# Optimization experiments

Hardware: AMD Instinct MI355X
Metric: run time of the kernel (lower is better)

## Reference

```python
import jax, jax.numpy as jnp
import numpy as np

NUM_HEADS = 16
ROPE_BASE = 10000.0


def _rope_cos_sin(seq_len, head_dim, dtype):
    inv_freq = 1.0 / (ROPE_BASE ** (jnp.arange(0, head_dim, 2, dtype=jnp.float32) / head_dim))
    freqs = jnp.arange(seq_len, dtype=jnp.float32)[:, None] * inv_freq[None, :]  # [L, hd/2]
    return jnp.cos(freqs).astype(dtype), jnp.sin(freqs).astype(dtype)


def _apply_rope(t, cos, sin):
    # t: [B, H, L, hd]; cos/sin: [L, hd/2] broadcast over B,H
    x1 = t[..., ::2]
    x2 = t[..., 1::2]
    r1 = x1 * cos - x2 * sin
    r2 = x1 * sin + x2 * cos
    return jnp.stack([r1, r2], axis=-1).reshape(t.shape)


def setup_inputs() -> dict:
    key = jax.random.key(0)
    k1, k2, k3 = jax.random.split(key, 3)
    B, L, D = 2, 2048, 1024
    x = jax.random.normal(k1, (B, L, D), dtype=jnp.float32)
    W_qkv = jax.random.normal(k2, (3 * D, D), dtype=jnp.float32) * (D ** -0.5)
    W_out = jax.random.normal(k3, (D, D), dtype=jnp.float32) * (D ** -0.5)
    return {"x": x, "W_qkv": W_qkv, "W_out": W_out}


def reference(x, W_qkv, W_out):
    B, L, D = x.shape
    H = NUM_HEADS
    hd = D // H
    scale = hd ** -0.5

    qkv = x @ W_qkv.T                              # [B, L, 3D]
    qkv = qkv.reshape(B, L, 3, H, hd)
    qkv = jnp.transpose(qkv, (2, 0, 3, 1, 4))      # [3, B, H, L, hd]
    q, k, v = qkv[0], qkv[1], qkv[2]

    cos, sin = _rope_cos_sin(L, hd, x.dtype)
    q = _apply_rope(q, cos, sin)
    k = _apply_rope(k, cos, sin)

    logits = jnp.einsum("bhqd,bhkd->bhqk", q, k) * scale
    attn = jax.nn.softmax(logits, axis=-1)         # dropout p=0.0 -> identity
    out = jnp.einsum("bhqk,bhkd->bhqd", attn, v)   # [B, H, L, hd]
    out = jnp.transpose(out, (0, 2, 1, 3)).reshape(B, L, D)
    return out @ W_out.T
```

## Files before the change

### kernel.cpp

```cpp
#include <hip/hip_runtime.h>
#include <hip/hip_bf16.h>
#include <stdint.h>


typedef __bf16 bf16x8 __attribute__((ext_vector_type(8)));
typedef float f32x4 __attribute__((ext_vector_type(4)));

__device__ __forceinline__ unsigned short f2bf(float f) {
  union { float f; unsigned int u; } v; v.f = f;
  unsigned int r = v.u + 0x7FFFu + ((v.u >> 16) & 1u);
  return (unsigned short)(r >> 16);
}
__device__ __forceinline__ float b2f(unsigned short u) {
  union { unsigned int u; float f; } v; v.u = ((unsigned int)u) << 16;
  return v.f;
}

__device__ __forceinline__ void gl2lds16(const void* gptr, void* lptr) {
  __builtin_amdgcn_global_load_lds(
      (const __attribute__((address_space(1))) unsigned int*)gptr,
      (__attribute__((address_space(3))) unsigned int*)lptr, 16, 0, 0);
}

__global__ void cvt_all(const float4* __restrict__ x,
                        const float4* __restrict__ wq,
                        const float4* __restrict__ wo,
                        ushort4* __restrict__ xb,
                        ushort4* __restrict__ wqb,
                        ushort4* __restrict__ wob,
                        float2* __restrict__ tab) {
  int i = blockIdx.x * 256 + threadIdx.x;
  if (i >= 2097152) {
    int t = i - 2097152;
    int l = t >> 5, fi = t & 31;
    float inv_freq = powf(10000.0f, -(float)fi / 32.0f);
    float s, c;
    sincosf((float)l * inv_freq, &s, &c);
    tab[t] = make_float2(c, s);
    return;
  }
  float4 v; ushort4* dst; int j;
  if (i < 1048576)      { v = x[i];            dst = xb;  j = i; }
  else if (i < 1835008) { v = wq[i - 1048576]; dst = wqb; j = i - 1048576; }
  else                  { v = wo[i - 1835008]; dst = wob; j = i - 1835008; }
  ushort4 o;
  o.x = f2bf(v.x); o.y = f2bf(v.y); o.z = f2bf(v.z); o.w = f2bf(v.w);
  dst[j] = o;
}

__global__ __launch_bounds__(256) void gemm1_fused(
    const __hip_bfloat16* __restrict__ A,
    const __hip_bfloat16* __restrict__ B,
    unsigned short* __restrict__ Qs,
    unsigned short* __restrict__ Ks,
    unsigned short* __restrict__ Vt,
    const float2* __restrict__ tab, int K) {
  __shared__ __align__(16) char lds[32768];
  const int tid = threadIdx.x;
  const int lane = tid & 63;
  const int wave = tid >> 6;
  const int wm = (wave >> 1) * 64, wn = (wave & 1) * 64;
  const int g = lane >> 4, lr = lane & 15;
  const int m0 = blockIdx.y * 128, n0 = blockIdx.x * 128;
  f32x4 acc[4][4] = {};

  const size_t ldb = (size_t)K * 2;
  const int c0 = tid, c1 = tid + 256;
  const int r0 = c0 >> 2, cb0 = ((c0 & 3) * 16) ^ (((r0 >> 1) & 3) << 4);
  const int r1 = c1 >> 2, cb1 = ((c1 & 3) * 16) ^ (((r1 >> 1) & 3) << 4);
  const char* A0 = (const char*)(A + (size_t)m0 * K) + (size_t)r0 * ldb + cb0;
  const char* A1 = (const char*)(A + (size_t)m0 * K) + (size_t)r1 * ldb + cb1;
  const char* B0 = (const char*)(B + (size_t)n0 * K) + (size_t)r0 * ldb + cb0;
  const char* B1 = (const char*)(B + (size_t)n0 * K) + (size_t)r1 * ldb + cb1;

  auto stage = [&](int bo) {
    gl2lds16(A0, lds + bo + c0 * 16);
    gl2lds16(A1, lds + bo + c1 * 16);
    gl2lds16(B0, lds + bo + 8192 + c0 * 16);
    gl2lds16(B1, lds + bo + 8192 + c1 * 16);
    A0 += 64; A1 += 64; B0 += 64; B1 += 64;
  };

  stage(0);

  const int swz = ((lr >> 1) & 3) << 4;
  const int NSTEP = K / 32;
  for (int kt = 0; kt < NSTEP; ++kt) {
    const int bo = (kt & 1) * 16384;
    if (kt + 1 < NSTEP) {
      stage(bo ^ 16384);
      asm volatile("s_waitcnt vmcnt(4)" ::: "memory");
    } else {
      asm volatile("s_waitcnt vmcnt(0)" ::: "memory");
    }
    __builtin_amdgcn_s_barrier();

    bf16x8 af[4], bfr[4];
#pragma unroll
    for (int i = 0; i < 4; ++i)
      af[i] = *(const bf16x8*)(lds + bo + (wm + i * 16 + lr) * 64 + ((g * 16) ^ swz));
#pragma unroll
    for (int i = 0; i < 4; ++i)
      bfr[i] = *(const bf16x8*)(lds + bo + 8192 + (wn + i * 16 + lr) * 64 + ((g * 16) ^ swz));
    __builtin_amdgcn_s_setprio(1);
#pragma unroll
    for (int i = 0; i < 4; ++i)
#pragma unroll
      for (int j = 0; j < 4; ++j)
        acc[i][j] = __builtin_amdgcn_mfma_f32_16x16x32_bf16(af[i], bfr[j], acc[i][j], 0, 0, 0);
    __builtin_amdgcn_s_setprio(0);
    asm volatile("s_waitcnt lgkmcnt(0)" ::: "memory");
    __builtin_amdgcn_s_barrier();
  }

  const int sel = n0 >> 10;
  if (sel <= 1) {
    const float qscale = (sel == 0) ? 0.125f * 1.44269504088896f : 1.0f;
    unsigned short* dst = (sel == 0) ? Qs : Ks;
#pragma unroll
    for (int j = 0; j < 4; ++j) {
      const int nn = (n0 + wn + j * 16 + lr) & 1023;
      const int h = nn >> 6, d = nn & 63;
      const float2* tabrow = tab + (d >> 1);
      const float sgn = (d & 1) ? 1.0f : -1.0f;
#pragma unroll
      for (int i = 0; i < 4; ++i) {
#pragma unroll
        for (int r = 0; r < 4; ++r) {
          const int m = m0 + wm + i * 16 + g * 4 + r;
          const int l = m & 2047, b = m >> 11;
          float own = acc[i][j][r];
          float part = __shfl_xor(own, 1);
          float2 cs = tabrow[l * 32];
          float out = fmaf(cs.x, own, sgn * cs.y * part) * qscale;
          dst[((size_t)((b * 16 + h) * 2048 + l)) * 64 + d] = f2bf(out);
        }
      }
    }
  } else {
#pragma unroll
    for (int j = 0; j < 4; ++j) {
      const int nn = (n0 + wn + j * 16 + lr) & 1023;
      const int h = nn >> 6, d = nn & 63;
#pragma unroll
      for (int i = 0; i < 4; ++i) {
        const int mb = m0 + wm + i * 16 + g * 4;
        const int l0 = mb & 2047, b = mb >> 11;
        const int pl = (l0 & ~31) + 8 * ((l0 & 15) >> 2) + 4 * ((l0 >> 4) & 1) + (l0 & 3);
        ushort4 v4;
        v4.x = f2bf(acc[i][j][0]); v4.y = f2bf(acc[i][j][1]);
        v4.z = f2bf(acc[i][j][2]); v4.w = f2bf(acc[i][j][3]);
        *(ushort4*)(Vt + ((size_t)((b * 16 + h) * 64 + d)) * 2048 + pl) = v4;
      }
    }
  }
}

__global__ __launch_bounds__(256) void gemm2_64(
    const __hip_bfloat16* __restrict__ A,
    const __hip_bfloat16* __restrict__ B,
    float* __restrict__ C, int M, int N, int K) {
  __shared__ __align__(16) char lds[16384];
  const int tid = threadIdx.x, lane = tid & 63, w = tid >> 6;
  const int g = lane >> 4, lr = lane & 15;
  const int n0 = blockIdx.x * 64, m0 = blockIdx.y * 64;
  f32x4 acc[4] = {};

  const size_t ld = (size_t)K * 2;
  const int o16 = tid * 16;
  const int s = o16 ^ (((o16 >> 7) & 3) << 4);
  const int srow = s >> 6, scolb = s & 63;
  const char* Asrc = (const char*)(A + (size_t)m0 * K) + (size_t)srow * ld + scolb;
  const char* Bsrc = (const char*)(B + (size_t)n0 * K) + (size_t)srow * ld + scolb;

  auto stage = [&](int bo) {
    gl2lds16(Asrc, lds + bo + o16);
    gl2lds16(Bsrc, lds + 8192 + bo + o16);
    Asrc += 64; Bsrc += 64;
  };

  stage(0);

  const int swz = ((lr >> 1) & 3) << 4;
  const int NSTEP = K / 32;
  for (int kt = 0; kt < NSTEP; ++kt) {
    const int bo = (kt & 1) * 4096;
    if (kt + 1 < NSTEP) {
      stage(bo ^ 4096);
      asm volatile("s_waitcnt vmcnt(2)" ::: "memory");
    } else {
      asm volatile("s_waitcnt vmcnt(0)" ::: "memory");
    }
    __builtin_amdgcn_s_barrier();

    bf16x8 af = *(const bf16x8*)(lds + bo + (w * 16 + lr) * 64 + ((g * 16) ^ swz));
    __builtin_amdgcn_s_setprio(1);
#pragma unroll
    for (int j = 0; j < 4; ++j) {
      bf16x8 bf = *(const bf16x8*)(lds + 8192 + bo + (j * 16 + lr) * 64 + ((g * 16) ^ swz));
      acc[j] = __builtin_amdgcn_mfma_f32_16x16x32_bf16(af, bf, acc[j], 0, 0, 0);
    }
    __builtin_amdgcn_s_setprio(0);
    asm volatile("s_waitcnt lgkmcnt(0)" ::: "memory");
    __builtin_amdgcn_s_barrier();
  }

#pragma unroll
  for (int j = 0; j < 4; ++j) {
    int n = n0 + j * 16 + lr;
#pragma unroll
    for (int r = 0; r < 4; ++r) {
      int m = m0 + w * 16 + g * 4 + r;
      C[(size_t)m * N + n] = acc[j][r];
    }
  }
}

__global__ __launch_bounds__(256, 4) void attn_fwd(
    const __hip_bfloat16* __restrict__ Qs,
    const __hip_bfloat16* __restrict__ Ks,
    const __hip_bfloat16* __restrict__ Vt,
    float* __restrict__ Opart,
    float2* __restrict__ Ml) {
  constexpr int L = 2048;
  __shared__ __align__(16) char lds[32768];
  const int tid = threadIdx.x, lane = tid & 63, w = tid >> 6;
  const int g = lane >> 4, lr = lane & 15;
  const int blk = blockIdx.x;
  const int xcd = blk & 7, slot = blk >> 3;
  const int bh = xcd * 4 + (slot >> 5);
  const int rem = slot & 31;
  const int qt = rem >> 1, half = rem & 1;
  const int q0 = qt * 128 + w * 32 + lr;
  const int kt0 = half * 16;

  const __hip_bfloat16* Qr = Qs + ((size_t)bh * L + q0) * 64;
  bf16x8 qf[2][2];
  qf[0][0] = *(const bf16x8*)(Qr + g * 8);
  qf[0][1] = *(const bf16x8*)(Qr + 32 + g * 8);
  qf[1][0] = *(const bf16x8*)(Qr + 16 * 64 + g * 8);
  qf[1][1] = *(const bf16x8*)(Qr + 16 * 64 + 32 + g * 8);

  bf16x8 onesf;
#pragma unroll
  for (int j = 0; j < 8; ++j) onesf[j] = (__bf16)1.0f;

  const int xmask = (lr & 7) << 4;
  const int loff0 = ((g * 16) ^ (xmask & 0x30)) + (xmask & 0x40);
  const int kb0 = lr * 128 + loff0;
  const int kb1 = kb0 ^ 64;

  const int c0 = tid * 16, c1 = c0 + 4096;
  const int os0 = c0 ^ (((c0 >> 7) & 7) << 4);
  const int os1 = c1 ^ (((c1 >> 7) & 7) << 4);
  const char* Kb = (const char*)(Ks + (size_t)bh * L * 64) + (size_t)kt0 * 8192;
  const char* Vb = (const char*)(Vt + (size_t)bh * 64 * L) + kt0 * 128;
  const char* KsrcA = Kb + os0;
  const char* KsrcB = Kb + os1;
  const char* VsrcA = Vb + (size_t)(os0 >> 7) * (L * 2) + (os0 & 127);
  const char* VsrcB = Vb + (size_t)(os1 >> 7) * (L * 2) + (os1 & 127);

  auto stage = [&](int bo) {
    gl2lds16(KsrcA, lds + bo + c0);
    gl2lds16(KsrcB, lds + bo + c1);
    gl2lds16(VsrcA, lds + 16384 + bo + c0);
    gl2lds16(VsrcB, lds + 16384 + bo + c1);
    KsrcA += 8192; KsrcB += 8192; VsrcA += 128; VsrcB += 128;
  };

  f32x4 oacc[2][4] = {};
  f32x4 lacc[2] = {};
  float mrun[2] = {-1e30f, -1e30f};

  stage(0);

  for (int kt = 0; kt < 16; ++kt) {
    const int bo = (kt & 1) * 8192;
    if (kt + 1 < 16) {
      stage(bo ^ 8192);
      asm volatile("s_waitcnt vmcnt(4)" ::: "memory");
    } else {
      asm volatile("s_waitcnt vmcnt(0)" ::: "memory");
    }
    __builtin_amdgcn_s_barrier();

    const char* Kc = lds + bo;
    const char* Vc = lds + 16384 + bo;

    f32x4 sacc[2][4] = {};
    __builtin_amdgcn_s_setprio(1);
#pragma unroll
    for (int mf = 0; mf < 4; ++mf) {
      bf16x8 a0 = *(const bf16x8*)(Kc + kb0 + mf * 2048);
      bf16x8 a1 = *(const bf16x8*)(Kc + kb1 + mf * 2048);
      sacc[0][mf] = __builtin_amdgcn_mfma_f32_16x16x32_bf16(a0, qf[0][0], sacc[0][mf], 0, 0, 0);
      sacc[0][mf] = __builtin_amdgcn_mfma_f32_16x16x32_bf16(a1, qf[0][1], sacc[0][mf], 0, 0, 0);
      sacc[1][mf] = __builtin_amdgcn_mfma_f32_16x16x32_bf16(a0, qf[1][0], sacc[1][mf], 0, 0, 0);
      sacc[1][mf] = __builtin_amdgcn_mfma_f32_16x16x32_bf16(a1, qf[1][1], sacc[1][mf], 0, 0, 0);
    }
    __builtin_amdgcn_s_setprio(0);

#pragma unroll
    for (int qg = 0; qg < 2; ++qg) {
      float a0 = fmaxf(fmaxf(sacc[qg][0][0], sacc[qg][0][1]), sacc[qg][0][2]);
      float a1 = fmaxf(fmaxf(sacc[qg][0][3], sacc[qg][1][0]), sacc[qg][1][1]);
      float a2 = fmaxf(fmaxf(sacc[qg][1][2], sacc[qg][1][3]), sacc[qg][2][0]);
      float a3 = fmaxf(fmaxf(sacc[qg][2][1], sacc[qg][2][2]), sacc[qg][2][3]);
      float a4 = fmaxf(fmaxf(sacc[qg][3][0], sacc[qg][3][1]), sacc[qg][3][2]);
      float b0 = fmaxf(fmaxf(a0, a1), a2);
      float b1 = fmaxf(fmaxf(a3, a4), sacc[qg][3][3]);
      float lmax = fmaxf(b0, b1);
      if (__any(lmax > mrun[qg] + 8.0f)) {
        float tmax = fmaxf(lmax, __shfl_xor(lmax, 16));
        tmax = fmaxf(tmax, __shfl_xor(tmax, 32));
        float mnew = fmaxf(mrun[qg], tmax);
        float al = __builtin_amdgcn_exp2f(mrun[qg] - mnew);
        mrun[qg] = mnew;
        lacc[qg] *= al;
#pragma unroll
        for (int d = 0; d < 4; ++d) oacc[qg][d] = oacc[qg][d] * al;
      }
#pragma unroll
      for (int mf = 0; mf < 4; ++mf) {
        sacc[qg][mf][0] = __builtin_amdgcn_exp2f(sacc[qg][mf][0] - mrun[qg]);
        sacc[qg][mf][1] = __builtin_amdgcn_exp2f(sacc[qg][mf][1] - mrun[qg]);
        sacc[qg][mf][2] = __builtin_amdgcn_exp2f(sacc[qg][mf][2] - mrun[qg]);
        sacc[qg][mf][3] = __builtin_amdgcn_exp2f(sacc[qg][mf][3] - mrun[qg]);
      }
    }

#pragma unroll
    for (int ks = 0; ks < 2; ++ks) {
      bf16x8 pf[2];
#pragma unroll
      for (int qg = 0; qg < 2; ++qg) {
#pragma unroll
        for (int j = 0; j < 4; ++j) {
          pf[qg][j]     = (__bf16)sacc[qg][2 * ks][j];
          pf[qg][4 + j] = (__bf16)sacc[qg][2 * ks + 1][j];
        }
      }
      const int kb = ks ? kb1 : kb0;
      __builtin_amdgcn_s_setprio(1);
      lacc[0] = __builtin_amdgcn_mfma_f32_16x16x32_bf16(onesf, pf[0], lacc[0], 0, 0, 0);
      lacc[1] = __builtin_amdgcn_mfma_f32_16x16x32_bf16(onesf, pf[1], lacc[1], 0, 0, 0);
#pragma unroll
      for (int df = 0; df < 4; ++df) {
        bf16x8 a = *(const bf16x8*)(Vc + kb + df * 2048);
        oacc[0][df] = __builtin_amdgcn_mfma_f32_16x16x32_bf16(a, pf[0], oacc[0][df], 0, 0, 0);
        oacc[1][df] = __builtin_amdgcn_mfma_f32_16x16x32_bf16(a, pf[1], oacc[1][df], 0, 0, 0);
      }
      __builtin_amdgcn_s_setprio(0);
    }
    asm volatile("s_waitcnt lgkmcnt(0)" ::: "memory");
    __builtin_amdgcn_s_barrier();
  }

#pragma unroll
  for (int qg = 0; qg < 2; ++qg) {
    const size_t rowi = ((size_t)bh * L + q0 + qg * 16) * 2 + half;
    float* Od = Opart + rowi * 64;
#pragma unroll
    for (int df = 0; df < 4; ++df)
      *(f32x4*)(Od + df * 16 + g * 4) = oacc[qg][df];
    if (g == 0) {
      float2 ml; ml.x = mrun[qg]; ml.y = lacc[qg][0];
      Ml[rowi] = ml;
    }
  }
}

__global__ __launch_bounds__(256) void attn_reduce(
    const float* __restrict__ Opart, const float2* __restrict__ Ml,
    unsigned short* __restrict__ Ob) {
  int t = blockIdx.x * 256 + threadIdx.x;
  int d = t & 63;
  int r = t >> 6;
  float2 a = Ml[2 * r], b = Ml[2 * r + 1];
  float m = fmaxf(a.x, b.x);
  float w0 = __builtin_amdgcn_exp2f(a.x - m);
  float w1 = __builtin_amdgcn_exp2f(b.x - m);
  float l = a.y * w0 + b.y * w1;
  float o = Opart[(size_t)(2 * r) * 64 + d] * w0 + Opart[(size_t)(2 * r + 1) * 64 + d] * w1;
  float out = o / l;
  int bh = r >> 11, qq = r & 2047;
  Ob[(((size_t)(bh >> 4) * 2048 + qq)) * 1024 + (bh & 15) * 64 + d] = f2bf(out);
}

extern "C" void kernel_launch(void* const* d_in, const int* in_sizes, int n_in,
                              void* d_out, int out_size, void* d_ws, size_t ws_size,
                              hipStream_t stream) {
  (void)in_sizes; (void)n_in; (void)out_size; (void)ws_size;
  const float* x    = (const float*)d_in[0];
  const float* wqkv = (const float*)d_in[1];
  const float* wout = (const float*)d_in[2];

  char* ws = (char*)d_ws;
  auto* wob   = (__hip_bfloat16*)(ws + ((size_t)0u  << 20));
  auto* Qsb   = (__hip_bfloat16*)(ws + ((size_t)2u  << 20));
  auto* Ob    = (__hip_bfloat16*)(ws + ((size_t)2u  << 20));
  auto* Ksb   = (__hip_bfloat16*)(ws + ((size_t)10u << 20));
  auto* Vtb   = (__hip_bfloat16*)(ws + ((size_t)18u << 20));
  auto* Opart = (float*)         (ws + ((size_t)26u << 20));
  auto* xb    = (__hip_bfloat16*)(ws + ((size_t)50u << 20));
  auto* Mlp   = (float2*)        (ws + ((size_t)58u << 20));
  auto* tab   = (float2*)        (ws + ((size_t)59u << 20));
  auto* wqb   = (__hip_bfloat16*)(ws + (((size_t)59u << 20) + ((size_t)1u << 19)));

  cvt_all<<<8448, 256, 0, stream>>>((const float4*)x, (const float4*)wqkv,
                                    (const float4*)wout,
                                    (ushort4*)xb, (ushort4*)wqb, (ushort4*)wob,
                                    tab);
  gemm1_fused<<<dim3(24, 32), 256, 0, stream>>>(xb, wqb,
                                                (unsigned short*)Qsb,
                                                (unsigned short*)Ksb,
                                                (unsigned short*)Vtb,
                                                tab, 1024);
  attn_fwd<<<1024, 256, 0, stream>>>(Qsb, Ksb, Vtb, Opart, Mlp);
  attn_reduce<<<16384, 256, 0, stream>>>(Opart, Mlp, (unsigned short*)Ob);
  gemm2_64<<<dim3(16, 64), 256, 0, stream>>>(Ob, wob, (float*)d_out,
                                             4096, 1024, 1024);
}
```

Measured before the change: 130.2 us.

## Shrink QKV GEMM tile to 128x64 and remap blocks per XCD

The QKV projection GEMM moves from 128x128 tiles on a 2D grid to 128x64 tiles on a 1D grid of 1536 blocks. Each wave now computes 32x64 instead of 64x64, and LDS per block drops to 24KB. Block IDs are decoded so that each of the 8 XCDs gets a contiguous M/N region, which aims to improve L2 reuse of A and B panels and to raise occupancy and block count. The cost is lower arithmetic intensity per block, so more global and LDS traffic per FLOP.

```diff
diff --git a/kernel.cpp b/kernel.cpp
--- a/kernel.cpp
+++ b/kernel.cpp
@@ -55,30 +55,33 @@
     unsigned short* __restrict__ Ks,
     unsigned short* __restrict__ Vt,
     const float2* __restrict__ tab, int K) {
-  __shared__ __align__(16) char lds[32768];
+  __shared__ __align__(16) char lds[24576];
   const int tid = threadIdx.x;
   const int lane = tid & 63;
-  const int wave = tid >> 6;
-  const int wm = (wave >> 1) * 64, wn = (wave & 1) * 64;
+  const int w = tid >> 6;
   const int g = lane >> 4, lr = lane & 15;
-  const int m0 = blockIdx.y * 128, n0 = blockIdx.x * 128;
-  f32x4 acc[4][4] = {};
+  const int bid = blockIdx.x;
+  const int xcd = bid & 7, idx = bid >> 3;
+  const int nt = idx % 24, mt = idx / 24;
+  const int m0 = (((xcd >> 1) << 3) + mt) * 128;
+  const int n0 = (((xcd & 1) * 24) + nt) * 64;
+  const int wm = w * 32;
+  f32x4 acc[2][4] = {};
 
   const size_t ldb = (size_t)K * 2;
-  const int c0 = tid, c1 = tid + 256;
-  const int r0 = c0 >> 2, cb0 = ((c0 & 3) * 16) ^ (((r0 >> 1) & 3) << 4);
-  const int r1 = c1 >> 2, cb1 = ((c1 & 3) * 16) ^ (((r1 >> 1) & 3) << 4);
-  const char* A0 = (const char*)(A + (size_t)m0 * K) + (size_t)r0 * ldb + cb0;
-  const char* A1 = (const char*)(A + (size_t)m0 * K) + (size_t)r1 * ldb + cb1;
-  const char* B0 = (const char*)(B + (size_t)n0 * K) + (size_t)r0 * ldb + cb0;
-  const char* B1 = (const char*)(B + (size_t)n0 * K) + (size_t)r1 * ldb + cb1;
+  const int ca0 = tid, ca1 = tid + 256, cb = tid;
+  const int ra0 = ca0 >> 2, sa0 = ((ca0 & 3) * 16) ^ (((ra0 >> 1) & 3) << 4);
+  const int ra1 = ca1 >> 2, sa1 = ((ca1 & 3) * 16) ^ (((ra1 >> 1) & 3) << 4);
+  const int rb  = cb  >> 2, sb  = ((cb  & 3) * 16) ^ (((rb  >> 1) & 3) << 4);
+  const char* A0 = (const char*)(A + (size_t)m0 * K) + (size_t)ra0 * ldb + sa0;
+  const char* A1 = (const char*)(A + (size_t)m0 * K) + (size_t)ra1 * ldb + sa1;
+  const char* B0 = (const char*)(B + (size_t)n0 * K) + (size_t)rb  * ldb + sb;
 
   auto stage = [&](int bo) {
-    gl2lds16(A0, lds + bo + c0 * 16);
-    gl2lds16(A1, lds + bo + c1 * 16);
-    gl2lds16(B0, lds + bo + 8192 + c0 * 16);
-    gl2lds16(B1, lds + bo + 8192 + c1 * 16);
-    A0 += 64; A1 += 64; B0 += 64; B1 += 64;
+    gl2lds16(A0, lds + bo + ca0 * 16);
+    gl2lds16(A1, lds + bo + ca1 * 16);
+    gl2lds16(B0, lds + bo + 8192 + cb * 16);
+    A0 += 64; A1 += 64; B0 += 64;
   };
 
   stage(0);
@@ -86,25 +89,25 @@
   const int swz = ((lr >> 1) & 3) << 4;
   const int NSTEP = K / 32;
   for (int kt = 0; kt < NSTEP; ++kt) {
-    const int bo = (kt & 1) * 16384;
+    const int bo = (kt & 1) * 12288;
     if (kt + 1 < NSTEP) {
-      stage(bo ^ 16384);
-      asm volatile("s_waitcnt vmcnt(4)" ::: "memory");
+      stage(bo ^ 12288);
+      asm volatile("s_waitcnt vmcnt(3)" ::: "memory");
     } else {
       asm volatile("s_waitcnt vmcnt(0)" ::: "memory");
     }
     __builtin_amdgcn_s_barrier();
 
-    bf16x8 af[4], bfr[4];
-#pragma unroll
-    for (int i = 0; i < 4; ++i)
+    bf16x8 af[2], bfr[4];
+#pragma unroll
+    for (int i = 0; i < 2; ++i)
       af[i] = *(const bf16x8*)(lds + bo + (wm + i * 16 + lr) * 64 + ((g * 16) ^ swz));
 #pragma unroll
-    for (int i = 0; i < 4; ++i)
-      bfr[i] = *(const bf16x8*)(lds + bo + 8192 + (wn + i * 16 + lr) * 64 + ((g * 16) ^ swz));
+    for (int j = 0; j < 4; ++j)
+      bfr[j] = *(const bf16x8*)(lds + bo + 8192 + (j * 16 + lr) * 64 + ((g * 16) ^ swz));
     __builtin_amdgcn_s_setprio(1);
 #pragma unroll
-    for (int i = 0; i < 4; ++i)
+    for (int i = 0; i < 2; ++i)
 #pragma unroll
       for (int j = 0; j < 4; ++j)
         acc[i][j] = __builtin_amdgcn_mfma_f32_16x16x32_bf16(af[i], bfr[j], acc[i][j], 0, 0, 0);
@@ -119,12 +122,12 @@
     unsigned short* dst = (sel == 0) ? Qs : Ks;
 #pragma unroll
     for (int j = 0; j < 4; ++j) {
-      const int nn = (n0 + wn + j * 16 + lr) & 1023;
+      const int nn = (n0 + j * 16 + lr) & 1023;
       const int h = nn >> 6, d = nn & 63;
       const float2* tabrow = tab + (d >> 1);
       const float sgn = (d & 1) ? 1.0f : -1.0f;
 #pragma unroll
-      for (int i = 0; i < 4; ++i) {
+      for (int i = 0; i < 2; ++i) {
 #pragma unroll
         for (int r = 0; r < 4; ++r) {
           const int m = m0 + wm + i * 16 + g * 4 + r;
@@ -140,10 +143,10 @@
   } else {
 #pragma unroll
     for (int j = 0; j < 4; ++j) {
-      const int nn = (n0 + wn + j * 16 + lr) & 1023;
+      const int nn = (n0 + j * 16 + lr) & 1023;
       const int h = nn >> 6, d = nn & 63;
 #pragma unroll
-      for (int i = 0; i < 4; ++i) {
+      for (int i = 0; i < 2; ++i) {
         const int mb = m0 + wm + i * 16 + g * 4;
         const int l0 = mb & 2047, b = mb >> 11;
         const int pl = (l0 & ~31) + 8 * ((l0 & 15) >> 2) + 4 * ((l0 >> 4) & 1) + (l0 & 3);
@@ -411,11 +414,11 @@
                                     (const float4*)wout,
                                     (ushort4*)xb, (ushort4*)wqb, (ushort4*)wob,
                                     tab);
-  gemm1_fused<<<dim3(24, 32), 256, 0, stream>>>(xb, wqb,
-                                                (unsigned short*)Qsb,
-                                                (unsigned short*)Ksb,
-                                                (unsigned short*)Vtb,
-                                                tab, 1024);
+  gemm1_fused<<<1536, 256, 0, stream>>>(xb, wqb,
+                                        (unsigned short*)Qsb,
+                                        (unsigned short*)Ksb,
+                                        (unsigned short*)Vtb,
+                                        tab, 1024);
   attn_fwd<<<1024, 256, 0, stream>>>(Qsb, Ksb, Vtb, Opart, Mlp);
   attn_reduce<<<16384, 256, 0, stream>>>(Opart, Mlp, (unsigned short*)Ob);
   gemm2_64<<<dim3(16, 64), 256, 0, stream>>>(Ob, wob, (float*)d_out,
```

Result: slower. 137.4 us (+5.5%).
